# Kernel tuning notes

Hardware: AMD Instinct MI355X
Metric: run time of the kernel (lower is better)

The kernel has to match this reference:

```python
import jax, jax.numpy as jnp
import numpy as np

D_SVG, N_TYPE, N_PAR = 256, 10, 12          # deep-svg latent, animation types, animation params
PADDING_VALUE = -1.0
W_SVG, W_TYPE, W_PAR = 10.0, 0.1, 1.0       # weight_deep_svg, weight_type, weight_parameters

# ANIMATION_PARAMETER_INDICES as a dense boolean lookup: type t -> which params it uses
_pm = np.zeros((N_TYPE, N_PAR), dtype=bool)
for _t in range(N_TYPE):
    for _k in (_t % N_PAR, (_t + 1) % N_PAR, (_t + 2) % N_PAR):
        _pm[_t, _k] = True
PARAM_MASK = jnp.asarray(_pm)


def setup_inputs() -> dict:
    B, S = 256, 512
    F = D_SVG + N_TYPE + N_PAR
    key = jax.random.key(0)
    k1, k2, k3, k4, k5 = jax.random.split(key, 5)
    x = jax.random.normal(k1, (B, S, F), dtype=jnp.float32)
    cls = jax.random.randint(k2, (B, S), 0, N_TYPE)
    t_type = jax.nn.one_hot(cls, N_TYPE, dtype=jnp.float32)
    t_svg = jax.random.normal(k3, (B, S, D_SVG), dtype=jnp.float32)
    t_par = jax.random.normal(k4, (B, S, N_PAR), dtype=jnp.float32)
    target = jnp.concatenate([t_svg, t_type, t_par], axis=-1)
    # suffix-contiguous padding (matches the `break` semantics of the torch loop)
    lengths = jax.random.randint(k5, (B,), S // 2, S + 1)
    mask = jnp.arange(S)[None, :] >= lengths[:, None]            # True = padded
    target = jnp.where(mask[..., None], PADDING_VALUE, target)
    return {"input": x, "target": target, "target_padding_mask": mask}


def reference(input, target, target_padding_mask):
    # input[expanded_mask] = -100
    x = jnp.where(target_padding_mask[..., None], -100.0, input)
    in_svg, in_type, in_par = jnp.split(x, [D_SVG, D_SVG + N_TYPE], axis=-1)
    tg_svg, tg_type, tg_par = jnp.split(target, [D_SVG, D_SVG + N_TYPE], axis=-1)

    valid = tg_type[..., 0] != PADDING_VALUE                      # [B,S] non-padded rows
    t_idx = jnp.argmax(tg_type, axis=-1)                          # [B,S] animation type

    # vectorized replacement of the double for-loop: copy target params at the
    # type-dependent ANIMATION_PARAMETER_INDICES into input params
    pmask = PARAM_MASK[t_idx] & valid[..., None]                  # [B,S,N_PAR]
    in_par = jnp.where(pmask, tg_par, in_par)

    # CrossEntropyLoss(ignore_index=-1) over flattened type logits
    logits = in_type.reshape(-1, N_TYPE)
    labels = t_idx.reshape(-1)
    v = valid.reshape(-1).astype(logits.dtype)
    logp = jax.nn.log_softmax(logits, axis=-1)
    nll = -jnp.take_along_axis(logp, labels[:, None], axis=1)[:, 0]
    loss_type = jnp.sum(nll * v) / jnp.maximum(jnp.sum(v), 1.0)

    # plain MSE (mean over ALL elements, padding included, as in the original)
    loss_svg = jnp.mean((in_svg - tg_svg) ** 2)
    loss_par = jnp.mean((in_par - tg_par) ** 2)

    return W_SVG * loss_svg + W_TYPE * loss_type + W_PAR * loss_par
```

## Files before the change

### kernel.cpp

```cpp
#include <hip/hip_runtime.h>
#include <math.h>

#define D_SVG 256
#define N_TYPE 10
#define N_PAR 12
#define F_TOT 278
#define ROWS_PER_BLOCK 64
#define THREADS 256
#define N4_PER_BLOCK (ROWS_PER_BLOCK * F_TOT / 4)
#define SECP 23
#define NXCD 8


__global__ __launch_bounds__(256) void bitmap_kernel(const float* __restrict__ target,
                                                     unsigned* __restrict__ bitmap) {
    const int tid = threadIdx.x;
    const long r = (long)blockIdx.x * 256 + tid;
    const bool valid = (target[r * F_TOT + D_SVG] != -1.0f);
    unsigned long long bal = __ballot(valid);
    const int lane = tid & 63, wv = tid >> 6;
    if (lane == 0)  bitmap[blockIdx.x * 8 + wv * 2]     = (unsigned)bal;
    if (lane == 32) bitmap[blockIdx.x * 8 + wv * 2 + 1] = (unsigned)(bal >> 32);
}

__global__ __launch_bounds__(THREADS, 2) void fused_kernel(const float* __restrict__ input,
                                                           const float* __restrict__ target,
                                                           const unsigned* __restrict__ bitmap,
                                                           float4* __restrict__ part,
                                                           int cpx) {
    __shared__ float s_in[ROWS_PER_BLOCK][SECP];
    __shared__ float s_tg[ROWS_PER_BLOCK][SECP];
    __shared__ float sred[4][4];
    const int tid  = threadIdx.x;
    const int lane = tid & 63, wave = tid >> 6;

    const int chunk = (blockIdx.x & (NXCD - 1)) * cpx + (blockIdx.x >> 3);

    const unsigned long long b = ((const unsigned long long*)bitmap)[chunk];

    if (b == 0ull) {
        if (tid == 0) part[chunk] = make_float4(0.f, 0.f, 0.f, 0.f);
        return;
    }

    const long row0 = (long)chunk * ROWS_PER_BLOCK;

    const unsigned k = (unsigned)__popcll(b);
    const unsigned long long pre = (k == 64u) ? ~0ull : ((1ull << k) - 1ull);
    const bool fast = (b == pre);
    const unsigned n4v = fast ? ((k * (unsigned)F_TOT + 3u) >> 2)
                              : (unsigned)N4_PER_BLOCK;

    const float4* __restrict__ in4p = (const float4*)(input  + row0 * F_TOT);
    const float4* __restrict__ tg4p = (const float4*)(target + row0 * F_TOT);

    float sall = 0.0f;

    if (fast) {
        unsigned idx = (unsigned)tid;
        for (; idx + 7u * THREADS < n4v; idx += 8u * THREADS) {
            float4 a[8], t[8];
            #pragma unroll
            for (int u = 0; u < 8; ++u) a[u] = in4p[idx + u * THREADS];
            #pragma unroll
            for (int u = 0; u < 8; ++u) t[u] = tg4p[idx + u * THREADS];
            #pragma unroll
            for (int u = 0; u < 8; ++u) {
                float dx = a[u].x - t[u].x, dy = a[u].y - t[u].y;
                float dz = a[u].z - t[u].z, dw = a[u].w - t[u].w;
                sall = fmaf(dx, dx, sall); sall = fmaf(dy, dy, sall);
                sall = fmaf(dz, dz, sall); sall = fmaf(dw, dw, sall);
            }
            __builtin_amdgcn_sched_group_barrier(0x020, 16, 0);
            __builtin_amdgcn_sched_group_barrier(0x002, 64, 0);
        }
        for (; idx < n4v; idx += THREADS) {
            float4 a = in4p[idx], t = tg4p[idx];
            float dx = a.x - t.x, dy = a.y - t.y, dz = a.z - t.z, dw = a.w - t.w;
            sall = fmaf(dx, dx, sall); sall = fmaf(dy, dy, sall);
            sall = fmaf(dz, dz, sall); sall = fmaf(dw, dw, sall);
        }
        if (tid == 0 && (k & 1u) && k < 64u) {
            const float* ip = input  + (row0 + k) * F_TOT;
            const float* tp = target + (row0 + k) * F_TOT;
            float d0 = ip[0] - tp[0], d1 = ip[1] - tp[1];
            sall -= d0 * d0 + d1 * d1;
        }
    } else {
        for (unsigned idx = (unsigned)tid; idx < (unsigned)N4_PER_BLOCK; idx += THREADS) {
            float4 a = in4p[idx], t = tg4p[idx];
            unsigned e0 = idx * 4u;
            unsigned ra = e0 / (unsigned)F_TOT;
            unsigned rb = (e0 + 2u) / (unsigned)F_TOT;
            float vA = (float)((unsigned)(b >> ra) & 1u);
            float vB = (float)((unsigned)(b >> rb) & 1u);
            float dx = a.x - t.x, dy = a.y - t.y, dz = a.z - t.z, dw = a.w - t.w;
            sall = fmaf(vA * dx, dx, sall); sall = fmaf(vA * dy, dy, sall);
            sall = fmaf(vB * dz, dz, sall); sall = fmaf(vB * dw, dw, sall);
        }
    }

    float stype = 0.0f, spar = 0.0f;
    {
        const int r = tid >> 2, c = tid & 3;
        if ((b >> r) & 1ull) {
            const float2* __restrict__ ip2 = (const float2*)(input  + (row0 + r) * F_TOT + D_SVG);
            const float2* __restrict__ tp2 = (const float2*)(target + (row0 + r) * F_TOT + D_SVG);
            #pragma unroll
            for (int m = 0; m < 3; ++m) {
                int j = c + 4 * m;
                if (j < 11) {
                    float2 iv = ip2[j], tv = tp2[j];
                    s_in[r][2*j] = iv.x; s_in[r][2*j + 1] = iv.y;
                    s_tg[r][2*j] = tv.x; s_tg[r][2*j + 1] = tv.y;
                    float d0 = iv.x - tv.x, d1 = iv.y - tv.y;
                    float sq = d0 * d0 + d1 * d1;
                    if (j < 5) stype += sq; else spar += sq;
                }
            }
        }
    }
    __syncthreads();

    float nll = 0.0f, corr = 0.0f;
    if (tid < ROWS_PER_BLOCK && ((b >> tid) & 1ull)) {
        float tt[N_TYPE], l[N_TYPE];
        #pragma unroll
        for (int j = 0; j < N_TYPE; ++j) { tt[j] = s_tg[tid][j]; l[j] = s_in[tid][j]; }
        int ti = 0; float best = tt[0];
        #pragma unroll
        for (int j = 1; j < N_TYPE; ++j) { if (tt[j] > best) { best = tt[j]; ti = j; } }
        float m = l[0];
        #pragma unroll
        for (int j = 1; j < N_TYPE; ++j) m = fmaxf(m, l[j]);
        float s = 0.0f;
        #pragma unroll
        for (int j = 0; j < N_TYPE; ++j) s += __expf(l[j] - m);
        nll = __logf(s) + m - l[ti];
        #pragma unroll
        for (int j = 0; j < 3; ++j) {
            float d = s_in[tid][N_TYPE + ti + j] - s_tg[tid][N_TYPE + ti + j];
            corr += d * d;
        }
    }

    float vals[4] = {sall - stype - spar, spar, nll, corr};
    #pragma unroll
    for (int v = 0; v < 4; ++v) {
        float x = vals[v];
        #pragma unroll
        for (int off = 32; off > 0; off >>= 1) x += __shfl_down(x, off, 64);
        vals[v] = x;
    }
    if (lane == 0) {
        #pragma unroll
        for (int v = 0; v < 4; ++v) sred[wave][v] = vals[v];
    }
    __syncthreads();
    if (tid == 0) {
        float s0 = sred[0][0] + sred[1][0] + sred[2][0] + sred[3][0];
        float s1 = sred[0][1] + sred[1][1] + sred[2][1] + sred[3][1];
        float s2 = sred[0][2] + sred[1][2] + sred[2][2] + sred[3][2];
        float s3 = sred[0][3] + sred[1][3] + sred[2][3] + sred[3][3];
        part[chunk] = make_float4(s0, s1, s2, s3);
    }
}

__global__ __launch_bounds__(256) void loss_final(const float4* __restrict__ part,
                                                  const unsigned* __restrict__ bitmap,
                                                  float* __restrict__ out,
                                                  int nb, int nw, int nrows) {
    __shared__ double sred[4][5];
    const int tid = threadIdx.x;
    double svg = 0.0, par = 0.0, nll = 0.0, corr = 0.0, cnt = 0.0;
    for (int i = tid; i < nb; i += 256) {
        float4 v = part[i];
        svg += v.x; par += v.y; nll += v.z; corr += v.w;
    }
    for (int i = tid; i < nw; i += 256)
        cnt += (double)__popc(bitmap[i]);
    double vals[5] = {svg, par, nll, corr, cnt};
    #pragma unroll
    for (int v = 0; v < 5; ++v) {
        double x = vals[v];
        #pragma unroll
        for (int off = 32; off > 0; off >>= 1) x += __shfl_down(x, off, 64);
        vals[v] = x;
    }
    const int wave = tid >> 6, lane = tid & 63;
    if (lane == 0) {
        #pragma unroll
        for (int v = 0; v < 5; ++v) sred[wave][v] = vals[v];
    }
    __syncthreads();
    if (tid == 0) {
        double S[5];
        #pragma unroll
        for (int v = 0; v < 5; ++v)
            S[v] = sred[0][v] + sred[1][v] + sred[2][v] + sred[3][v];
        double npad = (double)nrows - S[4];
        double svg_t = S[0] + 9801.0 * D_SVG * npad;
        double par_t = S[1] - S[3] + 9801.0 * N_PAR * npad;
        double loss = 10.0 * svg_t / ((double)nrows * D_SVG)
                    + 0.1  * S[2] / fmax(S[4], 1.0)
                    + 1.0  * par_t / ((double)nrows * N_PAR);
        out[0] = (float)loss;
    }
}

extern "C" void kernel_launch(void* const* d_in, const int* in_sizes, int n_in,
                              void* d_out, int out_size, void* d_ws, size_t ws_size,
                              hipStream_t stream) {
    const float* input  = (const float*)d_in[0];
    const float* target = (const float*)d_in[1];
    float* out = (float*)d_out;

    const int nrows = in_sizes[0] / F_TOT;
    const int blk   = nrows / ROWS_PER_BLOCK;
    const int nw    = nrows / 32;
    const int blk_m = nrows / 256;
    const int cpx   = blk / NXCD;

    float4*   part   = (float4*)d_ws;
    unsigned* bitmap = (unsigned*)((char*)d_ws + (size_t)blk * sizeof(float4));

    bitmap_kernel<<<blk_m, 256, 0, stream>>>(target, bitmap);
    fused_kernel<<<blk, THREADS, 0, stream>>>(input, target, bitmap, part, cpx);
    loss_final<<<1, 256, 0, stream>>>(part, bitmap, out, blk, nw, nrows);
}
```

Before: 298.1 us.

## Pipeline fast-path loads through LDS with async global_load_lds ring buffer

Replaces the register-unrolled 8-wide load loop in the all-valid fast path with a 4-stage ring buffer. Each wave issues direct global-to-LDS 16-byte loads and waits on vmcnt before consuming a stage, so memory traffic overlaps with compute. This is meant to keep more bytes in flight while using fewer VGPRs. The launch bounds drop the min-2-blocks hint, and the extra LDS and hand-written waitcnt sequencing add occupancy and correctness risks, including clamped redundant loads past the end.

After: 302.8 us. Within noise of the previous version (+1.6%).

```diff
diff --git a/kernel.cpp b/kernel.cpp
--- a/kernel.cpp
+++ b/kernel.cpp
@@ -10,6 +10,7 @@
 #define N4_PER_BLOCK (ROWS_PER_BLOCK * F_TOT / 4)
 #define SECP 23
 #define NXCD 8
+#define PIPE 4
 
 
 __global__ __launch_bounds__(256) void bitmap_kernel(const float* __restrict__ target,
@@ -23,11 +24,18 @@
     if (lane == 32) bitmap[blockIdx.x * 8 + wv * 2 + 1] = (unsigned)(bal >> 32);
 }
 
-__global__ __launch_bounds__(THREADS, 2) void fused_kernel(const float* __restrict__ input,
-                                                           const float* __restrict__ target,
-                                                           const unsigned* __restrict__ bitmap,
-                                                           float4* __restrict__ part,
-                                                           int cpx) {
+__device__ __forceinline__ void gload16(const float4* gp, float4* lbase) {
+    __builtin_amdgcn_global_load_lds(
+        (const __attribute__((address_space(1))) unsigned int*)gp,
+        (__attribute__((address_space(3))) unsigned int*)lbase, 16, 0, 0);
+}
+
+__global__ __launch_bounds__(THREADS) void fused_kernel(const float* __restrict__ input,
+                                                        const float* __restrict__ target,
+                                                        const unsigned* __restrict__ bitmap,
+                                                        float4* __restrict__ part,
+                                                        int cpx) {
+    __shared__ float4 stg[4][PIPE][2][64];
     __shared__ float s_in[ROWS_PER_BLOCK][SECP];
     __shared__ float s_tg[ROWS_PER_BLOCK][SECP];
     __shared__ float sred[4][4];
@@ -57,29 +65,34 @@
     float sall = 0.0f;
 
     if (fast) {
-        unsigned idx = (unsigned)tid;
-        for (; idx + 7u * THREADS < n4v; idx += 8u * THREADS) {
-            float4 a[8], t[8];
-            #pragma unroll
-            for (int u = 0; u < 8; ++u) a[u] = in4p[idx + u * THREADS];
-            #pragma unroll
-            for (int u = 0; u < 8; ++u) t[u] = tg4p[idx + u * THREADS];
-            #pragma unroll
-            for (int u = 0; u < 8; ++u) {
-                float dx = a[u].x - t[u].x, dy = a[u].y - t[u].y;
-                float dz = a[u].z - t[u].z, dw = a[u].w - t[u].w;
-                sall = fmaf(dx, dx, sall); sall = fmaf(dy, dy, sall);
-                sall = fmaf(dz, dz, sall); sall = fmaf(dw, dw, sall);
-            }
-            __builtin_amdgcn_sched_group_barrier(0x020, 16, 0);
-            __builtin_amdgcn_sched_group_barrier(0x002, 64, 0);
-        }
-        for (; idx < n4v; idx += THREADS) {
-            float4 a = in4p[idx], t = tg4p[idx];
-            float dx = a.x - t.x, dy = a.y - t.y, dz = a.z - t.z, dw = a.w - t.w;
+        const unsigned nst = (n4v + 255u) >> 8;
+
+        #pragma unroll
+        for (int s = 0; s < PIPE; ++s) {
+            unsigned idx = (unsigned)(s * 256 + tid);
+            unsigned ci  = (idx < n4v) ? idx : (n4v - 1u);
+            gload16(in4p + ci, &stg[wave][s][0][0]);
+            gload16(tg4p + ci, &stg[wave][s][1][0]);
+        }
+
+        for (unsigned i = 0; i < nst; ++i) {
+            asm volatile("s_waitcnt vmcnt(6)" ::: "memory");
+            float4 a = stg[wave][i & (PIPE - 1)][0][lane];
+            float4 t = stg[wave][i & (PIPE - 1)][1][lane];
+            unsigned idx = i * 256u + (unsigned)tid;
+            float msk = (idx < n4v) ? 1.0f : 0.0f;
+            float dx = (a.x - t.x) * msk, dy = (a.y - t.y) * msk;
+            float dz = (a.z - t.z) * msk, dw = (a.w - t.w) * msk;
             sall = fmaf(dx, dx, sall); sall = fmaf(dy, dy, sall);
             sall = fmaf(dz, dz, sall); sall = fmaf(dw, dw, sall);
-        }
+            asm volatile("s_waitcnt lgkmcnt(0)" ::: "memory");
+            unsigned nidx = (i + PIPE) * 256u + (unsigned)tid;
+            unsigned ci   = (nidx < n4v) ? nidx : (n4v - 1u);
+            gload16(in4p + ci, &stg[wave][i & (PIPE - 1)][0][0]);
+            gload16(tg4p + ci, &stg[wave][i & (PIPE - 1)][1][0]);
+        }
+        asm volatile("s_waitcnt vmcnt(0)" ::: "memory");
+
         if (tid == 0 && (k & 1u) && k < 64u) {
             const float* ip = input  + (row0 + k) * F_TOT;
             const float* tp = target + (row0 + k) * F_TOT;
```
